# Kernel optimization log

Hardware: AMD Instinct MI355X
Metric: run time of the kernel (lower is better)

## Reference

```python
import jax, jax.numpy as jnp
import numpy as np

EMBED_DIM = 1024
N_HEADS = 16
HEAD_DIM = EMBED_DIM // N_HEADS


def setup_inputs() -> dict:
    key = jax.random.key(0)
    ks = jax.random.split(key, 9)
    s = 1.0 / np.sqrt(EMBED_DIM)
    x = jax.random.normal(ks[0], (4, 2048, EMBED_DIM), dtype=jnp.float32)
    Wq = jax.random.uniform(ks[1], (EMBED_DIM, EMBED_DIM), jnp.float32, -s, s)
    bq = jax.random.uniform(ks[2], (EMBED_DIM,), jnp.float32, -s, s)
    Wk = jax.random.uniform(ks[3], (EMBED_DIM, EMBED_DIM), jnp.float32, -s, s)
    bk = jax.random.uniform(ks[4], (EMBED_DIM,), jnp.float32, -s, s)
    Wv = jax.random.uniform(ks[5], (EMBED_DIM, EMBED_DIM), jnp.float32, -s, s)
    bv = jax.random.uniform(ks[6], (EMBED_DIM,), jnp.float32, -s, s)
    Wo = jax.random.uniform(ks[7], (EMBED_DIM, EMBED_DIM), jnp.float32, -s, s)
    bo = jax.random.uniform(ks[8], (EMBED_DIM,), jnp.float32, -s, s)
    return {"x": x, "Wq": Wq, "bq": bq, "Wk": Wk, "bk": bk,
            "Wv": Wv, "bv": bv, "Wo": Wo, "bo": bo}


def reference(x, Wq, bq, Wk, bk, Wv, bv, Wo, bo):
    B, S, _ = x.shape
    # projections (PyTorch Linear: x @ W.T + b; weights stored as [in,out] here)
    q = x @ Wq + bq
    k = x @ Wk + bk
    v = x @ Wv + bv
    # [B, H, S, D]
    q = q.reshape(B, S, N_HEADS, HEAD_DIM).transpose(0, 2, 1, 3)
    k = k.reshape(B, S, N_HEADS, HEAD_DIM).transpose(0, 2, 1, 3)
    v = v.reshape(B, S, N_HEADS, HEAD_DIM).transpose(0, 2, 1, 3)
    scores = jnp.einsum('bhsd,bhtd->bhst', q, k) / np.sqrt(HEAD_DIM).astype(np.float32)
    attn = jax.nn.softmax(scores, axis=-1)
    out = jnp.einsum('bhst,bhtd->bhsd', attn, v)
    out = out.transpose(0, 2, 1, 3).reshape(B, S, EMBED_DIM)
    return out @ Wo + bo  # dropout=0 (eval) -> identity
```

## Files before the change

kernel.cpp:

```cpp
#include <hip/hip_runtime.h>
#include <stdint.h>

#define EMBED 1024
#define NH 16
#define HD 64
#define SEQ 2048
#define BATCH 4
#define M_TOT (BATCH*SEQ)
#define QSCALE 0.18033688011112042f

typedef __attribute__((ext_vector_type(8))) short short8;
typedef __attribute__((ext_vector_type(4))) float floatx4;
typedef __attribute__((ext_vector_type(4))) unsigned int uintx4;

__device__ __forceinline__ unsigned short f2bf(float f) {
    union { float f; unsigned int u; } v; v.f = f;
    unsigned int r = v.u + 0x7fffu + ((v.u >> 16) & 1u);
    return (unsigned short)(r >> 16);
}

__device__ __forceinline__ void load_lds16(const unsigned short* g, unsigned short* l) {
    __builtin_amdgcn_global_load_lds(
        (const __attribute__((address_space(1))) unsigned int*)g,
        (__attribute__((address_space(3))) unsigned int*)l, 16, 0, 0);
}

__global__ void cvt_x(const float* __restrict__ x, unsigned short* __restrict__ xb) {
    int i = (blockIdx.x * 256 + threadIdx.x) * 4;
    float4 v = *(const float4*)(x + i);
    ushort4 o;
    o.x = f2bf(v.x); o.y = f2bf(v.y); o.z = f2bf(v.z); o.w = f2bf(v.w);
    *(ushort4*)(xb + i) = o;
}

__global__ void wtrans(const float* __restrict__ w0, const float* __restrict__ w1,
                       const float* __restrict__ w2, const float* __restrict__ w3,
                       unsigned short* __restrict__ t0, unsigned short* __restrict__ t1,
                       unsigned short* __restrict__ t2, unsigned short* __restrict__ t3) {
    __shared__ float tile[32][33];
    const float* W; unsigned short* T;
    switch (blockIdx.z) { case 0: W=w0; T=t0; break; case 1: W=w1; T=t1; break;
                          case 2: W=w2; T=t2; break; default: W=w3; T=t3; }
    int n0 = blockIdx.x * 32, k0 = blockIdx.y * 32;
    int tx = threadIdx.x, ty = threadIdx.y;
    #pragma unroll
    for (int i = 0; i < 4; i++)
        tile[ty + i*8][tx] = W[(k0 + ty + i*8) * EMBED + n0 + tx];
    __syncthreads();
    #pragma unroll
    for (int i = 0; i < 4; i++)
        T[(n0 + ty + i*8) * EMBED + k0 + tx] = f2bf(tile[tx][ty + i*8]);
}

#define ST_A(buf_, kt_) do { \
    const unsigned short* s_ = Asrc + (kt_)*64; \
    unsigned short* d_ = ldst + (buf_)*32768; \
    load_lds16(s_,              d_); \
    load_lds16(s_ + 64*EMBED,   d_ + 4096); \
    load_lds16(s_ + 128*EMBED,  d_ + 8192); \
    load_lds16(s_ + 192*EMBED,  d_ + 12288); \
  } while(0)
#define ST_B(buf_, kt_, h_) do { \
    const unsigned short* s_ = Bsrc + (kt_)*64 + (h_)*128*EMBED; \
    unsigned short* d_ = ldst + (buf_)*32768 + 16384 + (h_)*8192; \
    load_lds16(s_,              d_); \
    load_lds16(s_ + 64*EMBED,   d_ + 4096); \
  } while(0)

__global__ __launch_bounds__(512, 2) void gemm8(
        const unsigned short* __restrict__ A, const unsigned short* __restrict__ BT,
        const float* __restrict__ b0, const float* __restrict__ b1, const float* __restrict__ b2,
        void* __restrict__ o0, void* __restrict__ o1, void* __restrict__ o2, int mode) {
    __shared__ unsigned short lds[2][2][256*64];
    const int tid = threadIdx.x;
    const int lane = tid & 63, wave = tid >> 6;
    const int quad = lane >> 4, l16 = lane & 15;
    const int wm = wave >> 2, wn = wave & 3;
    const int id = blockIdx.x;
    const int xcd = id & 7, j = id >> 3;
    const int mblk = (xcd * 4 + (j & 3)) * 256;
    const int nblk = (j >> 2) * 256;

    const int srow = tid >> 3;
    const int scol = ((tid & 7) ^ (srow & 7)) * 8;
    const unsigned short* Asrc = A  + (size_t)(mblk + srow) * EMBED + scol;
    const unsigned short* Bsrc = BT + (size_t)(nblk + srow) * EMBED + scol;
    unsigned short* ldst = &lds[0][0][0] + wave * 512;

    const int cs0 = ( quad      ^ (l16 & 7)) * 8;
    const int cs1 = ((quad ^ 4) ^ (l16 & 7)) * 8;
    const unsigned short* Abase = &lds[0][0][0] + (wm*128 + l16)*64;
    const unsigned short* Bbase = &lds[0][1][0] + (wn*64  + l16)*64;

    floatx4 acc[8][4];
    #pragma unroll
    for (int m=0;m<8;m++)
      #pragma unroll
      for (int n=0;n<4;n++) acc[m][n] = (floatx4){0.f,0.f,0.f,0.f};

    ST_A(0,0); ST_B(0,0,0); ST_B(0,0,1);
    ST_A(1,1);
    asm volatile("s_waitcnt vmcnt(4)" ::: "memory");
    __builtin_amdgcn_s_barrier();

    #pragma unroll 2
    for (int t = 0; t < 16; ++t) {
        const int buf = t & 1;
        const unsigned short* Ab = Abase + buf*32768;
        const unsigned short* Bb = Bbase + buf*32768;
        short8 fA[4][2], fBlo[2][2], fBhi[2][2];
        #pragma unroll
        for (int i=0;i<4;i++) {
            fA[i][0] = *(const short8*)(Ab + i*1024 + cs0);
            fA[i][1] = *(const short8*)(Ab + i*1024 + cs1);
        }
        #pragma unroll
        for (int n=0;n<2;n++) {
            fBlo[n][0] = *(const short8*)(Bb + n*1024 + cs0);
            fBlo[n][1] = *(const short8*)(Bb + n*1024 + cs1);
        }
        if (t < 15) ST_B(buf^1, t+1, 0);
        __builtin_amdgcn_s_barrier();
        asm volatile("s_waitcnt lgkmcnt(0)");
        __builtin_amdgcn_s_setprio(1);
        #pragma unroll
        for (int m=0;m<4;m++)
          #pragma unroll
          for (int n=0;n<2;n++) {
            acc[m][n] = __builtin_amdgcn_mfma_f32_16x16x32_bf16(fA[m][0], fBlo[n][0], acc[m][n], 0,0,0);
            acc[m][n] = __builtin_amdgcn_mfma_f32_16x16x32_bf16(fA[m][1], fBlo[n][1], acc[m][n], 0,0,0);
          }
        __builtin_amdgcn_s_setprio(0);
        __builtin_amdgcn_s_barrier();
        #pragma unroll
        for (int n=0;n<2;n++) {
            fBhi[n][0] = *(const short8*)(Bb + (2+n)*1024 + cs0);
            fBhi[n][1] = *(const short8*)(Bb + (2+n)*1024 + cs1);
        }
        if (t < 15) ST_B(buf^1, t+1, 1);
        __builtin_amdgcn_s_barrier();
        asm volatile("s_waitcnt lgkmcnt(0)");
        __builtin_amdgcn_s_setprio(1);
        #pragma unroll
        for (int m=0;m<4;m++)
          #pragma unroll
          for (int n=0;n<2;n++) {
            acc[m][2+n] = __builtin_amdgcn_mfma_f32_16x16x32_bf16(fA[m][0], fBhi[n][0], acc[m][2+n], 0,0,0);
            acc[m][2+n] = __builtin_amdgcn_mfma_f32_16x16x32_bf16(fA[m][1], fBhi[n][1], acc[m][2+n], 0,0,0);
          }
        __builtin_amdgcn_s_setprio(0);
        __builtin_amdgcn_s_barrier();
        #pragma unroll
        for (int i=0;i<4;i++) {
            fA[i][0] = *(const short8*)(Ab + (4+i)*1024 + cs0);
            fA[i][1] = *(const short8*)(Ab + (4+i)*1024 + cs1);
        }
        __builtin_amdgcn_s_barrier();
        asm volatile("s_waitcnt lgkmcnt(0)");
        __builtin_amdgcn_s_setprio(1);
        #pragma unroll
        for (int m=0;m<4;m++)
          #pragma unroll
          for (int n=0;n<2;n++) {
            acc[4+m][2+n] = __builtin_amdgcn_mfma_f32_16x16x32_bf16(fA[m][0], fBhi[n][0], acc[4+m][2+n], 0,0,0);
            acc[4+m][2+n] = __builtin_amdgcn_mfma_f32_16x16x32_bf16(fA[m][1], fBhi[n][1], acc[4+m][2+n], 0,0,0);
          }
        __builtin_amdgcn_s_setprio(0);
        __builtin_amdgcn_s_barrier();
        if (t < 14) ST_A(buf, t+2);
        __builtin_amdgcn_s_setprio(1);
        #pragma unroll
        for (int m=0;m<4;m++)
          #pragma unroll
          for (int n=0;n<2;n++) {
            acc[4+m][n] = __builtin_amdgcn_mfma_f32_16x16x32_bf16(fA[m][0], fBlo[n][0], acc[4+m][n], 0,0,0);
            acc[4+m][n] = __builtin_amdgcn_mfma_f32_16x16x32_bf16(fA[m][1], fBlo[n][1], acc[4+m][n], 0,0,0);
          }
        __builtin_amdgcn_s_setprio(0);
        if (t < 14)       { asm volatile("s_waitcnt vmcnt(4)" ::: "memory"); }
        else if (t == 14) { asm volatile("s_waitcnt vmcnt(0)" ::: "memory"); }
        __builtin_amdgcn_s_barrier();
    }

    if (mode == 1) {
        float* O = (float*)o0;
        #pragma unroll
        for (int mt=0;mt<8;mt++)
          #pragma unroll
          for (int nt=0;nt<4;nt++) {
            int col = nblk + wn*64 + nt*16 + l16;
            float bv = b0[col];
            #pragma unroll
            for (int r=0;r<4;r++) {
                int row = mblk + wm*128 + mt*16 + quad*4 + r;
                O[(size_t)row * EMBED + col] = acc[mt][nt][r] + bv;
            }
          }
    } else {
        int which = nblk >> 10;
        const float* bs = (which==0) ? b0 : (which==1) ? b1 : b2;
        unsigned short* O = (unsigned short*)((which==0) ? o0 : (which==1) ? o1 : o2);
        #pragma unroll
        for (int mt=0;mt<8;mt++)
          #pragma unroll
          for (int nt=0;nt<4;nt++) {
            int coll = (nblk & 1023) + wn*64 + nt*16 + l16;
            float bv = bs[coll];
            int h = coll >> 6, d = coll & 63;
            #pragma unroll
            for (int r=0;r<4;r++) {
                int row = mblk + wm*128 + mt*16 + quad*4 + r;
                int b = row >> 11, s = row & 2047;
                float v = acc[mt][nt][r] + bv;
                if (which == 0) {
                    v *= QSCALE;
                    O[((size_t)(b*NH + h)*SEQ + s)*HD + d] = f2bf(v);
                } else if (which == 1) {
                    O[((size_t)(b*NH + h)*SEQ + s)*HD + d] = f2bf(v);
                } else {
                    int sp = (s & ~31) | (((s >> 2) & 3) << 3) | (((s >> 4) & 1) << 2) | (s & 3);
                    O[((size_t)(b*NH + h)*HD + d)*SEQ + sp] = f2bf(v);
                }
            }
          }
    }
}

__global__ __launch_bounds__(512, 4) void attn(
    const unsigned short* __restrict__ Q, const unsigned short* __restrict__ K,
    const unsigned short* __restrict__ VTp, unsigned short* __restrict__ O) {
    __shared__ unsigned short kv[4096];
    int tid = threadIdx.x;
    int lane = tid & 63, wave = tid >> 6;
    int quad = lane >> 4, l16 = lane & 15;
    int id = blockIdx.x;
    int bh = (id & 7) * 8 + (id >> 6);
    int qblk = (id >> 3) & 7;
    int b = bh >> 4, h = bh & 15;
    int q0 = qblk * 256 + wave * 32;
    const unsigned short* Qb = Q + (size_t)bh * SEQ * HD;
    const unsigned short* Kb = K + (size_t)bh * SEQ * HD;
    const unsigned short* Vb = VTp + (size_t)bh * HD * SEQ;
    int li = (wave & 3) * 64 + lane;
    const unsigned short* src;
    unsigned short* dst = kv + (wave & 3) * 512 + ((wave >> 2) ? 2048 : 0);
    int src_step;
    if (wave < 4) {
        int t = li >> 3, slot = li & 7;
        int dblk = slot ^ (t & 7);
        src = Kb + (size_t)t * HD + dblk * 8;
        src_step = 32 * HD;
    } else {
        int d = li >> 2, slot = li & 3;
        int swz = (d & 3) ^ ((d >> 2) & 3);
        src = Vb + (size_t)d * SEQ + (slot ^ swz) * 8;
        src_step = 32;
    }
    short8 qf[2][2];
    #pragma unroll
    for (int mt=0;mt<2;mt++) {
        const unsigned short* qp = Qb + (size_t)(q0 + mt*16 + l16) * HD + quad*8;
        qf[mt][0] = *(const short8*)(qp);
        qf[mt][1] = *(const short8*)(qp + 32);
    }
    floatx4 o_acc[2][4], l_acc[2];
    #pragma unroll
    for (int mt=0;mt<2;mt++) {
        l_acc[mt] = (floatx4){0.f,0.f,0.f,0.f};
        #pragma unroll
        for (int dt=0;dt<4;dt++) o_acc[mt][dt] = (floatx4){0.f,0.f,0.f,0.f};
    }
    short8 ones;
    #pragma unroll
    for (int jj=0;jj<8;jj++) ones[jj] = (short)0x3F80;
    int koff[2][2], voff[4];
    #pragma unroll
    for (int nt=0;nt<2;nt++) {
        int t = nt*16 + l16;
        #pragma unroll
        for (int hh=0;hh<2;hh++)
            koff[nt][hh] = t*64 + ((hh*4 + quad) ^ (t & 7)) * 8;
    }
    #pragma unroll
    for (int dt=0;dt<4;dt++) {
        int d = dt*16 + l16;
        voff[dt] = 2048 + d*32 + ((quad ^ (d & 3) ^ ((d >> 2) & 3))) * 8;
    }

    for (int tb = 0; tb < SEQ; tb += 32) {
        load_lds16(src, dst);
        src += src_step;
        __syncthreads();
        short8 kf[2][2], vf[4];
        #pragma unroll
        for (int nt=0;nt<2;nt++) {
            kf[nt][0] = *(const short8*)(kv + koff[nt][0]);
            kf[nt][1] = *(const short8*)(kv + koff[nt][1]);
        }
        #pragma unroll
        for (int dt=0;dt<4;dt++)
            vf[dt] = *(const short8*)(kv + voff[dt]);
        floatx4 sacc[2][2];
        #pragma unroll
        for (int nt=0;nt<2;nt++)
          #pragma unroll
          for (int mt=0;mt<2;mt++) {
            floatx4 s = (floatx4){0.f,0.f,0.f,0.f};
            s = __builtin_amdgcn_mfma_f32_16x16x32_bf16(kf[nt][0], qf[mt][0], s, 0, 0, 0);
            s = __builtin_amdgcn_mfma_f32_16x16x32_bf16(kf[nt][1], qf[mt][1], s, 0, 0, 0);
            sacc[nt][mt] = s;
          }
        short8 pf[2];
        #pragma unroll
        for (int mt=0;mt<2;mt++) {
            uintx4 pu;
            #pragma unroll
            for (int jp=0;jp<4;jp++) {
                int nt = jp >> 1, rp = (jp & 1) * 2;
                union { float f; unsigned int u; } e0, e1;
                e0.f = __builtin_amdgcn_exp2f(sacc[nt][mt][rp]);
                e1.f = __builtin_amdgcn_exp2f(sacc[nt][mt][rp+1]);
                pu[jp] = ((e1.u + 0x8000u) & 0xFFFF0000u) | ((e0.u + 0x8000u) >> 16);
            }
            pf[mt] = __builtin_bit_cast(short8, pu);
        }
        #pragma unroll
        for (int mt=0;mt<2;mt++) {
            l_acc[mt] = __builtin_amdgcn_mfma_f32_16x16x32_bf16(ones, pf[mt], l_acc[mt], 0, 0, 0);
            #pragma unroll
            for (int dt=0;dt<4;dt++)
                o_acc[mt][dt] = __builtin_amdgcn_mfma_f32_16x16x32_bf16(vf[dt], pf[mt], o_acc[mt][dt], 0, 0, 0);
        }
        __syncthreads();
    }
    #pragma unroll
    for (int mt=0;mt<2;mt++) {
        float inv = 1.f / l_acc[mt][0];
        int s = q0 + mt*16 + l16;
        #pragma unroll
        for (int dt=0;dt<4;dt++) {
            ushort4 w;
            w.x = f2bf(o_acc[mt][dt][0]*inv);
            w.y = f2bf(o_acc[mt][dt][1]*inv);
            w.z = f2bf(o_acc[mt][dt][2]*inv);
            w.w = f2bf(o_acc[mt][dt][3]*inv);
            *(ushort4*)(O + ((size_t)b*SEQ + s)*EMBED + h*HD + dt*16 + quad*4) = w;
        }
    }
}

extern "C" void kernel_launch(void* const* d_in, const int* in_sizes, int n_in,
                              void* d_out, int out_size, void* d_ws, size_t ws_size,
                              hipStream_t stream) {
    const float* x  = (const float*)d_in[0];
    const float* Wq = (const float*)d_in[1]; const float* bq = (const float*)d_in[2];
    const float* Wk = (const float*)d_in[3]; const float* bk = (const float*)d_in[4];
    const float* Wv = (const float*)d_in[5]; const float* bv = (const float*)d_in[6];
    const float* Wo = (const float*)d_in[7]; const float* bo = (const float*)d_in[8];
    char* ws = (char*)d_ws;
    unsigned short* xb  = (unsigned short*)(ws);
    unsigned short* WqT = (unsigned short*)(ws + (16ull<<20));
    unsigned short* WkT = (unsigned short*)(ws + (18ull<<20));
    unsigned short* WvT = (unsigned short*)(ws + (20ull<<20));
    unsigned short* WoT = (unsigned short*)(ws + (22ull<<20));
    unsigned short* Qb  = (unsigned short*)(ws + (24ull<<20));
    unsigned short* Kb  = (unsigned short*)(ws + (40ull<<20));
    unsigned short* VTb = (unsigned short*)(ws + (56ull<<20));
    unsigned short* Ob  = xb;

    cvt_x<<<(M_TOT*EMBED)/1024, 256, 0, stream>>>(x, xb);
    wtrans<<<dim3(32,32,4), dim3(32,8), 0, stream>>>(Wq,Wk,Wv,Wo, WqT,WkT,WvT,WoT);
    gemm8<<<dim3(384), 512, 0, stream>>>(xb, WqT, bq, bk, bv, Qb, Kb, VTb, 0);
    attn<<<dim3(512), 512, 0, stream>>>(Qb, Kb, VTb, Ob);
    gemm8<<<dim3(128), 512, 0, stream>>>(Ob, WoT, bo, bo, bo, (float*)d_out, nullptr, nullptr, 1);
}
```

Before: 296.8 us.

## Rebalance GEMM LDS staging across phases and double-buffer attention K/V tiles

The GEMM main loop is split into a templated per-k-tile helper that spreads the A and B global-to-LDS loads into smaller half-tile chunks across the four MFMA phases, with a reworked B row mapping and finer vmcnt/lgkmcnt waits. The attention kernel gains a second K/V LDS buffer, so the next tile's load is issued before computing the current one, replacing the two full syncthreads with a vmcnt wait plus a barrier. MFMA blocks are also wrapped in setprio. The aim is to hide global-load latency behind MFMA work, at the cost of more LDS per attention block and a more fragile hand-written wait-count schedule.

```diff
diff --git a/kernel.cpp b/kernel.cpp
--- a/kernel.cpp
+++ b/kernel.cpp
@@ -52,26 +52,96 @@
         T[(n0 + ty + i*8) * EMBED + k0 + tx] = f2bf(tile[tx][ty + i*8]);
 }
 
-#define ST_A(buf_, kt_) do { \
-    const unsigned short* s_ = Asrc + (kt_)*64; \
-    unsigned short* d_ = ldst + (buf_)*32768; \
+#define ST_AH(buf_, kt_, h_) do { \
+    const unsigned short* s_ = Asrc + (kt_)*64 + (h_)*64*EMBED; \
+    unsigned short* d_ = ldst + (buf_)*32768 + (h_)*4096; \
     load_lds16(s_,              d_); \
-    load_lds16(s_ + 64*EMBED,   d_ + 4096); \
     load_lds16(s_ + 128*EMBED,  d_ + 8192); \
-    load_lds16(s_ + 192*EMBED,  d_ + 12288); \
   } while(0)
-#define ST_B(buf_, kt_, h_) do { \
-    const unsigned short* s_ = Bsrc + (kt_)*64 + (h_)*128*EMBED; \
-    unsigned short* d_ = ldst + (buf_)*32768 + 16384 + (h_)*8192; \
+#define ST_BH(buf_, kt_, h_) do { \
+    const unsigned short* s_ = Bsrc + (kt_)*64 + (h_)*32*EMBED; \
+    unsigned short* d_ = bdst + (buf_)*32768 + (h_)*2048; \
     load_lds16(s_,              d_); \
-    load_lds16(s_ + 64*EMBED,   d_ + 4096); \
+    load_lds16(s_ + 128*EMBED,  d_ + 8192); \
   } while(0)
+
+template<int MO, int NO>
+__device__ __forceinline__ void mfma_quad(floatx4 (&acc)[8][4],
+        const short8 (&a)[4][2], const short8 (&b)[2][2]) {
+    #pragma unroll
+    for (int k=0;k<2;k++)
+      #pragma unroll
+      for (int m=0;m<4;m++)
+        #pragma unroll
+        for (int n=0;n<2;n++)
+          acc[MO+m][NO+n] = __builtin_amdgcn_mfma_f32_16x16x32_bf16(a[m][k], b[n][k], acc[MO+m][NO+n], 0,0,0);
+}
+
+template<bool B1, bool T2, int WAITN>
+__device__ __forceinline__ void ktile(int t, int buf,
+        const unsigned short* Abase, const unsigned short* Bbase,
+        const unsigned short* Asrc, const unsigned short* Bsrc,
+        unsigned short* ldst, unsigned short* bdst,
+        int cs0, int cs1, floatx4 (&acc)[8][4]) {
+    const unsigned short* Ab = Abase + buf*32768;
+    const unsigned short* Bb = Bbase + buf*32768;
+    short8 fA[4][2], fBlo[2][2], fBhi[2][2];
+    #pragma unroll
+    for (int i=0;i<4;i++) {
+        fA[i][0] = *(const short8*)(Ab + i*1024 + cs0);
+        fA[i][1] = *(const short8*)(Ab + i*1024 + cs1);
+    }
+    #pragma unroll
+    for (int n=0;n<2;n++) {
+        fBlo[n][0] = *(const short8*)(Bb + n*1024 + cs0);
+        fBlo[n][1] = *(const short8*)(Bb + n*1024 + cs1);
+    }
+    if (B1) ST_BH(buf^1, t+1, 1);
+    asm volatile("s_waitcnt lgkmcnt(8)");
+    __builtin_amdgcn_s_barrier();
+    asm volatile("s_waitcnt lgkmcnt(0)");
+    __builtin_amdgcn_s_setprio(1);
+    mfma_quad<0,0>(acc, fA, fBlo);
+    __builtin_amdgcn_s_setprio(0);
+    __builtin_amdgcn_s_barrier();
+    #pragma unroll
+    for (int n=0;n<2;n++) {
+        fBhi[n][0] = *(const short8*)(Bb + (2+n)*1024 + cs0);
+        fBhi[n][1] = *(const short8*)(Bb + (2+n)*1024 + cs1);
+    }
+    if (T2) ST_AH(buf, t+2, 0);
+    __builtin_amdgcn_s_barrier();
+    asm volatile("s_waitcnt lgkmcnt(0)");
+    __builtin_amdgcn_s_setprio(1);
+    mfma_quad<0,2>(acc, fA, fBhi);
+    __builtin_amdgcn_s_setprio(0);
+    __builtin_amdgcn_s_barrier();
+    #pragma unroll
+    for (int i=0;i<4;i++) {
+        fA[i][0] = *(const short8*)(Ab + (4+i)*1024 + cs0);
+        fA[i][1] = *(const short8*)(Ab + (4+i)*1024 + cs1);
+    }
+    if (T2) ST_BH(buf, t+2, 0);
+    __builtin_amdgcn_s_barrier();
+    asm volatile("s_waitcnt lgkmcnt(0)");
+    __builtin_amdgcn_s_setprio(1);
+    mfma_quad<4,2>(acc, fA, fBhi);
+    __builtin_amdgcn_s_setprio(0);
+    __builtin_amdgcn_s_barrier();
+    if (T2) ST_AH(buf, t+2, 1);
+    __builtin_amdgcn_s_setprio(1);
+    mfma_quad<4,0>(acc, fA, fBlo);
+    __builtin_amdgcn_s_setprio(0);
+    if (WAITN == 6)      { asm volatile("s_waitcnt vmcnt(6)" ::: "memory"); }
+    else if (WAITN == 0) { asm volatile("s_waitcnt vmcnt(0)" ::: "memory"); }
+    __builtin_amdgcn_s_barrier();
+}
 
 __global__ __launch_bounds__(512, 2) void gemm8(
         const unsigned short* __restrict__ A, const unsigned short* __restrict__ BT,
         const float* __restrict__ b0, const float* __restrict__ b1, const float* __restrict__ b2,
         void* __restrict__ o0, void* __restrict__ o1, void* __restrict__ o2, int mode) {
-    __shared__ unsigned short lds[2][2][256*64];
+    __shared__ unsigned short lds[2*32768];
     const int tid = threadIdx.x;
     const int lane = tid & 63, wave = tid >> 6;
     const int quad = lane >> 4, l16 = lane & 15;
@@ -83,14 +153,16 @@
 
     const int srow = tid >> 3;
     const int scol = ((tid & 7) ^ (srow & 7)) * 8;
+    const int brow = (srow & 31) + ((srow >> 5) << 6);
     const unsigned short* Asrc = A  + (size_t)(mblk + srow) * EMBED + scol;
-    const unsigned short* Bsrc = BT + (size_t)(nblk + srow) * EMBED + scol;
-    unsigned short* ldst = &lds[0][0][0] + wave * 512;
+    const unsigned short* Bsrc = BT + (size_t)(nblk + brow) * EMBED + scol;
+    unsigned short* ldst = lds + wave * 512;
+    unsigned short* bdst = lds + 16384 + (wave & 3)*512 + (wave >> 2)*4096;
 
     const int cs0 = ( quad      ^ (l16 & 7)) * 8;
     const int cs1 = ((quad ^ 4) ^ (l16 & 7)) * 8;
-    const unsigned short* Abase = &lds[0][0][0] + (wm*128 + l16)*64;
-    const unsigned short* Bbase = &lds[0][1][0] + (wn*64  + l16)*64;
+    const unsigned short* Abase = lds + (wm*128 + l16)*64;
+    const unsigned short* Bbase = lds + 16384 + (wn*64 + l16)*64;
 
     floatx4 acc[8][4];
     #pragma unroll
@@ -98,89 +170,17 @@
       #pragma unroll
       for (int n=0;n<4;n++) acc[m][n] = (floatx4){0.f,0.f,0.f,0.f};
 
-    ST_A(0,0); ST_B(0,0,0); ST_B(0,0,1);
-    ST_A(1,1);
+    ST_AH(0,0,0); ST_BH(0,0,0); ST_BH(0,0,1); ST_AH(0,0,1);
     asm volatile("s_waitcnt vmcnt(4)" ::: "memory");
+    ST_AH(1,1,0); ST_BH(1,1,0); ST_AH(1,1,1);
+    asm volatile("s_waitcnt vmcnt(6)" ::: "memory");
     __builtin_amdgcn_s_barrier();
 
     #pragma unroll 2
-    for (int t = 0; t < 16; ++t) {
-        const int buf = t & 1;
-        const unsigned short* Ab = Abase + buf*32768;
-        const unsigned short* Bb = Bbase + buf*32768;
-        short8 fA[4][2], fBlo[2][2], fBhi[2][2];
-        #pragma unroll
-        for (int i=0;i<4;i++) {
-            fA[i][0] = *(const short8*)(Ab + i*1024 + cs0);
-            fA[i][1] = *(const short8*)(Ab + i*1024 + cs1);
-        }
-        #pragma unroll
-        for (int n=0;n<2;n++) {
-            fBlo[n][0] = *(const short8*)(Bb + n*1024 + cs0);
-            fBlo[n][1] = *(const short8*)(Bb + n*1024 + cs1);
-        }
-        if (t < 15) ST_B(buf^1, t+1, 0);
-        __builtin_amdgcn_s_barrier();
-        asm volatile("s_waitcnt lgkmcnt(0)");
-        __builtin_amdgcn_s_setprio(1);
-        #pragma unroll
-        for (int m=0;m<4;m++)
-          #pragma unroll
-          for (int n=0;n<2;n++) {
-            acc[m][n] = __builtin_amdgcn_mfma_f32_16x16x32_bf16(fA[m][0], fBlo[n][0], acc[m][n], 0,0,0);
-            acc[m][n] = __builtin_amdgcn_mfma_f32_16x16x32_bf16(fA[m][1], fBlo[n][1], acc[m][n], 0,0,0);
-          }
-        __builtin_amdgcn_s_setprio(0);
-        __builtin_amdgcn_s_barrier();
-        #pragma unroll
-        for (int n=0;n<2;n++) {
-            fBhi[n][0] = *(const short8*)(Bb + (2+n)*1024 + cs0);
-            fBhi[n][1] = *(const short8*)(Bb + (2+n)*1024 + cs1);
-        }
-        if (t < 15) ST_B(buf^1, t+1, 1);
-        __builtin_amdgcn_s_barrier();
-        asm volatile("s_waitcnt lgkmcnt(0)");
-        __builtin_amdgcn_s_setprio(1);
-        #pragma unroll
-        for (int m=0;m<4;m++)
-          #pragma unroll
-          for (int n=0;n<2;n++) {
-            acc[m][2+n] = __builtin_amdgcn_mfma_f32_16x16x32_bf16(fA[m][0], fBhi[n][0], acc[m][2+n], 0,0,0);
-            acc[m][2+n] = __builtin_amdgcn_mfma_f32_16x16x32_bf16(fA[m][1], fBhi[n][1], acc[m][2+n], 0,0,0);
-          }
-        __builtin_amdgcn_s_setprio(0);
-        __builtin_amdgcn_s_barrier();
-        #pragma unroll
-        for (int i=0;i<4;i++) {
-            fA[i][0] = *(const short8*)(Ab + (4+i)*1024 + cs0);
-            fA[i][1] = *(const short8*)(Ab + (4+i)*1024 + cs1);
-        }
-        __builtin_amdgcn_s_barrier();
-        asm volatile("s_waitcnt lgkmcnt(0)");
-        __builtin_amdgcn_s_setprio(1);
-        #pragma unroll
-        for (int m=0;m<4;m++)
-          #pragma unroll
-          for (int n=0;n<2;n++) {
-            acc[4+m][2+n] = __builtin_amdgcn_mfma_f32_16x16x32_bf16(fA[m][0], fBhi[n][0], acc[4+m][2+n], 0,0,0);
-            acc[4+m][2+n] = __builtin_amdgcn_mfma_f32_16x16x32_bf16(fA[m][1], fBhi[n][1], acc[4+m][2+n], 0,0,0);
-          }
-        __builtin_amdgcn_s_setprio(0);
-        __builtin_amdgcn_s_barrier();
-        if (t < 14) ST_A(buf, t+2);
-        __builtin_amdgcn_s_setprio(1);
-        #pragma unroll
-        for (int m=0;m<4;m++)
-          #pragma unroll
-          for (int n=0;n<2;n++) {
-            acc[4+m][n] = __builtin_amdgcn_mfma_f32_16x16x32_bf16(fA[m][0], fBlo[n][0], acc[4+m][n], 0,0,0);
-            acc[4+m][n] = __builtin_amdgcn_mfma_f32_16x16x32_bf16(fA[m][1], fBlo[n][1], acc[4+m][n], 0,0,0);
-          }
-        __builtin_amdgcn_s_setprio(0);
-        if (t < 14)       { asm volatile("s_waitcnt vmcnt(4)" ::: "memory"); }
-        else if (t == 14) { asm volatile("s_waitcnt vmcnt(0)" ::: "memory"); }
-        __builtin_amdgcn_s_barrier();
-    }
+    for (int t = 0; t < 14; ++t)
+        ktile<true, true, 6>(t, t & 1, Abase, Bbase, Asrc, Bsrc, ldst, bdst, cs0, cs1, acc);
+    ktile<true,  false, 0>(14, 0, Abase, Bbase, Asrc, Bsrc, ldst, bdst, cs0, cs1, acc);
+    ktile<false, false, -1>(15, 1, Abase, Bbase, Asrc, Bsrc, ldst, bdst, cs0, cs1, acc);
 
     if (mode == 1) {
         float* O = (float*)o0;
@@ -229,7 +229,8 @@
 __global__ __launch_bounds__(512, 4) void attn(
     const unsigned short* __restrict__ Q, const unsigned short* __restrict__ K,
     const unsigned short* __restrict__ VTp, unsigned short* __restrict__ O) {
-    __shared__ unsigned short kv[4096];
+    __shared__ unsigned short kv[2][4096];
+    unsigned short* kvf = &kv[0][0];
     int tid = threadIdx.x;
     int lane = tid & 63, wave = tid >> 6;
     int quad = lane >> 4, l16 = lane & 15;
@@ -243,7 +244,7 @@
     const unsigned short* Vb = VTp + (size_t)bh * HD * SEQ;
     int li = (wave & 3) * 64 + lane;
     const unsigned short* src;
-    unsigned short* dst = kv + (wave & 3) * 512 + ((wave >> 2) ? 2048 : 0);
+    int dstofs = (wave & 3) * 512 + ((wave >> 2) ? 2048 : 0);
     int src_step;
     if (wave < 4) {
         int t = li >> 3, slot = li & 7;
@@ -287,20 +288,31 @@
         voff[dt] = 2048 + d*32 + ((quad ^ (d & 3) ^ ((d >> 2) & 3))) * 8;
     }
 
-    for (int tb = 0; tb < SEQ; tb += 32) {
-        load_lds16(src, dst);
-        src += src_step;
-        __syncthreads();
+    load_lds16(src, kvf + dstofs);
+    src += src_step;
+
+    for (int it = 0; it < 64; ++it) {
+        const unsigned short* kb = kvf + (it & 1) * 4096;
+        if (it < 63) {
+            load_lds16(src, kvf + ((it & 1) ^ 1) * 4096 + dstofs);
+            src += src_step;
+            asm volatile("s_waitcnt vmcnt(1)" ::: "memory");
+        } else {
+            asm volatile("s_waitcnt vmcnt(0)" ::: "memory");
+        }
+        __builtin_amdgcn_s_barrier();
+        asm volatile("" ::: "memory");
         short8 kf[2][2], vf[4];
         #pragma unroll
         for (int nt=0;nt<2;nt++) {
-            kf[nt][0] = *(const short8*)(kv + koff[nt][0]);
-            kf[nt][1] = *(const short8*)(kv + koff[nt][1]);
+            kf[nt][0] = *(const short8*)(kb + koff[nt][0]);
+            kf[nt][1] = *(const short8*)(kb + koff[nt][1]);
         }
         #pragma unroll
         for (int dt=0;dt<4;dt++)
-            vf[dt] = *(const short8*)(kv + voff[dt]);
+            vf[dt] = *(const short8*)(kb + voff[dt]);
         floatx4 sacc[2][2];
+        __builtin_amdgcn_s_setprio(1);
         #pragma unroll
         for (int nt=0;nt<2;nt++)
           #pragma unroll
@@ -310,6 +322,7 @@
             s = __builtin_amdgcn_mfma_f32_16x16x32_bf16(kf[nt][1], qf[mt][1], s, 0, 0, 0);
             sacc[nt][mt] = s;
           }
+        __builtin_amdgcn_s_setprio(0);
         short8 pf[2];
         #pragma unroll
         for (int mt=0;mt<2;mt++) {
@@ -324,6 +337,7 @@
             }
             pf[mt] = __builtin_bit_cast(short8, pu);
         }
+        __builtin_amdgcn_s_setprio(1);
         #pragma unroll
         for (int mt=0;mt<2;mt++) {
             l_acc[mt] = __builtin_amdgcn_mfma_f32_16x16x32_bf16(ones, pf[mt], l_acc[mt], 0, 0, 0);
@@ -331,7 +345,9 @@
             for (int dt=0;dt<4;dt++)
                 o_acc[mt][dt] = __builtin_amdgcn_mfma_f32_16x16x32_bf16(vf[dt], pf[mt], o_acc[mt][dt], 0, 0, 0);
         }
-        __syncthreads();
+        __builtin_amdgcn_s_setprio(0);
+        asm volatile("" ::: "memory");
+        __builtin_amdgcn_s_barrier();
     }
     #pragma unroll
     for (int mt=0;mt<2;mt++) {
```

Result: faster. 289.1 us (-2.6%).
